# Performance work log

Hardware: AMD Instinct MI355X
Metric: run time of the kernel (lower is better)

Reference implementation:

```python
import jax, jax.numpy as jnp
import numpy as np

N_NODES = 10000
DEG = 32          # random neighbors per node; +1 self loop (A + I in original)
BATCH = 2
F_IN = 128
D_EMB = 128


def _make_edges():
    # np.where on a dense (A+I) matrix yields edges sorted by source row;
    # we build the same sorted-by-src edge list directly.
    rng = np.random.default_rng(0)
    src = np.repeat(np.arange(N_NODES), DEG + 1)
    dst = rng.integers(0, N_NODES, size=N_NODES * (DEG + 1))
    dst[DEG::DEG + 1] = np.arange(N_NODES)  # guarantee self loops
    return np.stack([src, dst], axis=1).astype(np.int32)  # [E, 2]


def setup_inputs() -> dict:
    key = jax.random.key(0)
    k1, k2, k3 = jax.random.split(key, 3)
    inputs = jax.random.normal(k1, (BATCH, N_NODES, F_IN), jnp.float32)
    W = jax.random.normal(k2, (F_IN, D_EMB), jnp.float32) * 0.1
    W_attn = jax.random.normal(k3, (2 * D_EMB, 1), jnp.float32) * 0.1
    edges = jnp.asarray(_make_edges())
    return {"inputs": inputs, "W": W, "W_attn": W_attn, "edges": edges}


def reference(inputs, W, W_attn, edges):
    # inputs: [B, N, F]; W: [F, D]; W_attn: [2D, 1]; edges: [E, 2] (sorted by src)
    B, N, _ = inputs.shape
    D = W.shape[1]
    src, dst = edges[:, 0], edges[:, 1]

    h = inputs @ W  # [B, N, D] node_states_transformed

    # Original: gather [src,dst] feats, reshape to [B,E,2D], matmul W_attn.
    # Equivalent efficient form: split W_attn and project per node first.
    a_src, a_dst = W_attn[:D, 0], W_attn[D:, 0]
    s = h @ a_src  # [B, N]
    d = h @ a_dst  # [B, N]
    scores = jax.nn.leaky_relu(s[:, src] + d[:, dst], negative_slope=0.2)  # [B, E]
    scores = jnp.exp(jnp.clip(scores, -2.0, 2.0))

    # Faithful to original bug: denominator uses batch 0 only, shared across batch.
    denom = jax.ops.segment_sum(scores[0], src, num_segments=N)  # [N]
    # edges sorted by src => tf.repeat(denom, bincount(src)) == denom[src]
    attn = scores / denom[src][None, :]  # [B, E]

    msgs = h[:, dst] * attn[:, :, None]  # [B, E, D]
    # tf.unsorted_segment_sum with rank-2 segment_ids sums over batch AND edges.
    out = jax.ops.segment_sum(msgs.sum(axis=0), src, num_segments=N)  # [N, D]
    return jnp.broadcast_to(out[None], (B, N, D))
```

## Files before the change

kernel.cpp:

```cpp
#include <hip/hip_runtime.h>
#include <math.h>

#define N_NODES 10000
#define DEG1 33
#define D_EMB 128
#define F_IN 128
#define BATCH 2

typedef short s8v  __attribute__((ext_vector_type(8)));
typedef float f4v  __attribute__((ext_vector_type(4)));

static __device__ __forceinline__ unsigned short f2bf(float f) {
    unsigned int x = __float_as_uint(f);
    unsigned int r = (x + 0x7fffu + ((x >> 16) & 1u)) >> 16;
    return (unsigned short)r;
}
static __device__ __forceinline__ float bf_lo(unsigned int u) { return __uint_as_float(u << 16); }
static __device__ __forceinline__ float bf_hi(unsigned int u) { return __uint_as_float(u & 0xffff0000u); }
static __device__ __forceinline__ float rdlane_f(float v, int l) {
    return __uint_as_float((unsigned int)__builtin_amdgcn_readlane((int)__float_as_uint(v), l));
}

__global__ __launch_bounds__(256) void gat_prep_kernel(
    const float* __restrict__ W, unsigned short* __restrict__ wtf)
{
    const int c = blockIdx.x;
    const int t = threadIdx.x;
    __shared__ float xs[128 * 16];
    #pragma unroll
    for (int r = 0; r < 8; ++r) {
        const int k = r * 16 + (t >> 4);
        const int n = t & 15;
        xs[k * 16 + n] = W[k * 128 + c * 16 + n];
    }
    __syncthreads();
    const int s = t >> 6;
    const int l = t & 63;
    s8v frag;
    #pragma unroll
    for (int j = 0; j < 8; ++j) {
        const int k = s * 32 + (l >> 4) * 8 + j;
        frag[j] = (short)f2bf(xs[k * 16 + (l & 15)]);
    }
    *(s8v*)&wtf[(((size_t)c * 4 + s) * 64 + l) * 8] = frag;
}

__global__ __launch_bounds__(256) void gat_h_kernel(
    const float* __restrict__ X, const unsigned short* __restrict__ wtf,
    const float* __restrict__ Wattn,
    unsigned short* __restrict__ hb, float* __restrict__ s_arr, float* __restrict__ d_arr)
{
    const int w = blockIdx.x * 4 + (threadIdx.x >> 6);
    if (w >= (BATCH * N_NODES) / 16) return;
    const int lane = threadIdx.x & 63;
    const int quad = lane >> 4;
    const int mrow = lane & 15;
    const int row0 = w * 16;

    f4v acc[8];
    #pragma unroll
    for (int c = 0; c < 8; ++c) acc[c] = (f4v){0.f, 0.f, 0.f, 0.f};

    const float* xrow = X + (size_t)(row0 + mrow) * F_IN;
    #pragma unroll
    for (int s = 0; s < 4; ++s) {
        const int k0 = s * 32 + quad * 8;
        const float4 xa = *(const float4*)&xrow[k0];
        const float4 xbv = *(const float4*)&xrow[k0 + 4];
        s8v a;
        a[0] = (short)f2bf(xa.x);  a[1] = (short)f2bf(xa.y);
        a[2] = (short)f2bf(xa.z);  a[3] = (short)f2bf(xa.w);
        a[4] = (short)f2bf(xbv.x); a[5] = (short)f2bf(xbv.y);
        a[6] = (short)f2bf(xbv.z); a[7] = (short)f2bf(xbv.w);
        #pragma unroll
        for (int c = 0; c < 8; ++c) {
            const s8v b = *(const s8v*)&wtf[(((size_t)c * 4 + s) * 64 + lane) * 8];
            acc[c] = __builtin_amdgcn_mfma_f32_16x16x32_bf16(a, b, acc[c], 0, 0, 0);
        }
    }

    const int b = (row0 >= N_NODES) ? 1 : 0;
    #pragma unroll
    for (int r = 0; r < 4; ++r) {
        const int R = row0 + quad * 4 + r;
        const int n = R - b * N_NODES;
        unsigned short* dst = &hb[((size_t)n * 2 + b) * D_EMB + mrow];
        #pragma unroll
        for (int c = 0; c < 8; ++c)
            dst[c * 16] = f2bf(acc[c][r]);
    }

    float as[8], ad[8];
    #pragma unroll
    for (int c = 0; c < 8; ++c) {
        as[c] = Wattn[c * 16 + mrow];
        ad[c] = Wattn[D_EMB + c * 16 + mrow];
    }
    #pragma unroll
    for (int r = 0; r < 4; ++r) {
        float sv = 0.f, dv = 0.f;
        #pragma unroll
        for (int c = 0; c < 8; ++c) {
            sv = fmaf(acc[c][r], as[c], sv);
            dv = fmaf(acc[c][r], ad[c], dv);
        }
        #pragma unroll
        for (int off = 1; off < 16; off <<= 1) {
            sv += __shfl_xor(sv, off, 16);
            dv += __shfl_xor(dv, off, 16);
        }
        if (mrow == 0) {
            const int R = row0 + quad * 4 + r;
            s_arr[R] = sv;
            d_arr[R] = dv;
        }
    }
}

__global__ __launch_bounds__(256) void gat_agg_kernel(
    const uint2* __restrict__ h2, const float* __restrict__ s_arr,
    const float* __restrict__ d_arr, const int* __restrict__ edges,
    float* __restrict__ out)
{
    const int i = blockIdx.x * 4 + (threadIdx.x >> 6);
    const int lane = threadIdx.x & 63;

    int dstv = 0; float sc0 = 0.f, sc1 = 0.f;
    if (lane < DEG1) {
        dstv = edges[((size_t)i * DEG1 + lane) * 2 + 1];
        float x0 = s_arr[i] + d_arr[dstv];
        float x1 = s_arr[N_NODES + i] + d_arr[N_NODES + dstv];
        x0 = (x0 >= 0.f) ? x0 : 0.2f * x0;
        x1 = (x1 >= 0.f) ? x1 : 0.2f * x1;
        sc0 = __expf(fminf(fmaxf(x0, -2.f), 2.f));
        sc1 = __expf(fminf(fmaxf(x1, -2.f), 2.f));
    }
    float dsum = sc0;
    #pragma unroll
    for (int off = 1; off < 64; off <<= 1) dsum += __shfl_xor(dsum, off, 64);
    const float inv = 1.f / dsum;
    sc0 *= inv;
    sc1 *= inv;

    float4 acc = make_float4(0.f, 0.f, 0.f, 0.f);
    #pragma unroll
    for (int j = 0; j < DEG1; ++j) {
        const int   dd = __builtin_amdgcn_readlane(dstv, j);
        const float w0 = rdlane_f(sc0, j);
        const float w1 = rdlane_f(sc1, j);
        const float wgt = (lane < 32) ? w0 : w1;
        const uint2 hv = h2[(size_t)dd * 64 + lane];
        acc.x = fmaf(wgt, bf_lo(hv.x), acc.x);
        acc.y = fmaf(wgt, bf_hi(hv.x), acc.y);
        acc.z = fmaf(wgt, bf_lo(hv.y), acc.z);
        acc.w = fmaf(wgt, bf_hi(hv.y), acc.w);
    }
    float4 o;
    o.x = acc.x + __shfl_xor(acc.x, 32, 64);
    o.y = acc.y + __shfl_xor(acc.y, 32, 64);
    o.z = acc.z + __shfl_xor(acc.z, 32, 64);
    o.w = acc.w + __shfl_xor(acc.w, 32, 64);

    const int b  = lane >> 5;
    const int dl = lane & 31;
    *(float4*)&out[((size_t)b * N_NODES + i) * D_EMB + dl * 4] = o;
}

extern "C" void kernel_launch(void* const* d_in, const int* in_sizes, int n_in,
                              void* d_out, int out_size, void* d_ws, size_t ws_size,
                              hipStream_t stream) {
    const float* X     = (const float*)d_in[0];
    const float* W     = (const float*)d_in[1];
    const float* Wattn = (const float*)d_in[2];
    const int*   edges = (const int*)d_in[3];
    float* out = (float*)d_out;

    unsigned short* wtf = (unsigned short*)d_ws;
    unsigned short* hb  = wtf + 16384;
    float* s_arr = (float*)(hb + (size_t)BATCH * N_NODES * D_EMB);
    float* d_arr = s_arr + BATCH * N_NODES;

    gat_prep_kernel<<<8, 256, 0, stream>>>(W, wtf);
    gat_h_kernel<<<313, 256, 0, stream>>>(X, wtf, Wattn, hb, s_arr, d_arr);
    gat_agg_kernel<<<N_NODES / 4, 256, 0, stream>>>((const uint2*)hb, s_arr, d_arr, edges, out);
}
```

Before: 90.52 us.

## Split feature table into column halves and aggregate in two passes

The bf16 node-feature table is now written as two separate tables, one per 64-column half. Aggregation runs as two launches, each gathering neighbor rows from one half-table and writing its half of the output columns. The aim is to shrink the randomly gathered working set per pass so it fits better in the per-XCD L2 cache. In exchange, edge loading, attention-score computation and softmax normalisation are done twice, each gather moves only 4 bytes per lane, and there is an extra kernel launch.

```diff
diff --git a/kernel.cpp b/kernel.cpp
--- a/kernel.cpp
+++ b/kernel.cpp
@@ -48,7 +48,8 @@
 __global__ __launch_bounds__(256) void gat_h_kernel(
     const float* __restrict__ X, const unsigned short* __restrict__ wtf,
     const float* __restrict__ Wattn,
-    unsigned short* __restrict__ hb, float* __restrict__ s_arr, float* __restrict__ d_arr)
+    unsigned short* __restrict__ hbA, unsigned short* __restrict__ hbB,
+    float* __restrict__ s_arr, float* __restrict__ d_arr)
 {
     const int w = blockIdx.x * 4 + (threadIdx.x >> 6);
     if (w >= (BATCH * N_NODES) / 16) return;
@@ -84,10 +85,12 @@
     for (int r = 0; r < 4; ++r) {
         const int R = row0 + quad * 4 + r;
         const int n = R - b * N_NODES;
-        unsigned short* dst = &hb[((size_t)n * 2 + b) * D_EMB + mrow];
+        const size_t base = ((size_t)n * 2 + b) * 64 + mrow;
         #pragma unroll
-        for (int c = 0; c < 8; ++c)
-            dst[c * 16] = f2bf(acc[c][r]);
+        for (int c = 0; c < 8; ++c) {
+            unsigned short* tab = (c < 4) ? hbA : hbB;
+            tab[base + (c & 3) * 16] = f2bf(acc[c][r]);
+        }
     }
 
     float as[8], ad[8];
@@ -117,10 +120,10 @@
     }
 }
 
-__global__ __launch_bounds__(256) void gat_agg_kernel(
-    const uint2* __restrict__ h2, const float* __restrict__ s_arr,
-    const float* __restrict__ d_arr, const int* __restrict__ edges,
-    float* __restrict__ out)
+__global__ __launch_bounds__(256) void gat_agg_half_kernel(
+    const unsigned int* __restrict__ tab,
+    const float* __restrict__ s_arr, const float* __restrict__ d_arr,
+    const int* __restrict__ edges, float* __restrict__ out, const int half)
 {
     const int i = blockIdx.x * 4 + (threadIdx.x >> 6);
     const int lane = threadIdx.x & 63;
@@ -142,28 +145,25 @@
     sc0 *= inv;
     sc1 *= inv;
 
-    float4 acc = make_float4(0.f, 0.f, 0.f, 0.f);
+    const int b  = lane >> 5;
+    const int dl = lane & 31;
+    float2 acc = make_float2(0.f, 0.f);
     #pragma unroll
     for (int j = 0; j < DEG1; ++j) {
         const int   dd = __builtin_amdgcn_readlane(dstv, j);
         const float w0 = rdlane_f(sc0, j);
         const float w1 = rdlane_f(sc1, j);
         const float wgt = (lane < 32) ? w0 : w1;
-        const uint2 hv = h2[(size_t)dd * 64 + lane];
-        acc.x = fmaf(wgt, bf_lo(hv.x), acc.x);
-        acc.y = fmaf(wgt, bf_hi(hv.x), acc.y);
-        acc.z = fmaf(wgt, bf_lo(hv.y), acc.z);
-        acc.w = fmaf(wgt, bf_hi(hv.y), acc.w);
+        const unsigned int u = tab[(((size_t)dd * 2 + b) << 5) + dl];
+        acc.x = fmaf(wgt, bf_lo(u), acc.x);
+        acc.y = fmaf(wgt, bf_hi(u), acc.y);
     }
-    float4 o;
+    float2 o;
     o.x = acc.x + __shfl_xor(acc.x, 32, 64);
     o.y = acc.y + __shfl_xor(acc.y, 32, 64);
-    o.z = acc.z + __shfl_xor(acc.z, 32, 64);
-    o.w = acc.w + __shfl_xor(acc.w, 32, 64);
 
-    const int b  = lane >> 5;
-    const int dl = lane & 31;
-    *(float4*)&out[((size_t)b * N_NODES + i) * D_EMB + dl * 4] = o;
+    float2* out2 = (float2*)out;
+    out2[((size_t)b * N_NODES + i) * (D_EMB / 2) + half * 32 + dl] = o;
 }
 
 extern "C" void kernel_launch(void* const* d_in, const int* in_sizes, int n_in,
@@ -176,11 +176,15 @@
     float* out = (float*)d_out;
 
     unsigned short* wtf = (unsigned short*)d_ws;
-    unsigned short* hb  = wtf + 16384;
-    float* s_arr = (float*)(hb + (size_t)BATCH * N_NODES * D_EMB);
+    unsigned short* hbA = wtf + 16384;
+    unsigned short* hbB = hbA + (size_t)BATCH * N_NODES * 64;
+    float* s_arr = (float*)(hbB + (size_t)BATCH * N_NODES * 64);
     float* d_arr = s_arr + BATCH * N_NODES;
 
     gat_prep_kernel<<<8, 256, 0, stream>>>(W, wtf);
-    gat_h_kernel<<<313, 256, 0, stream>>>(X, wtf, Wattn, hb, s_arr, d_arr);
-    gat_agg_kernel<<<N_NODES / 4, 256, 0, stream>>>((const uint2*)hb, s_arr, d_arr, edges, out);
+    gat_h_kernel<<<313, 256, 0, stream>>>(X, wtf, Wattn, hbA, hbB, s_arr, d_arr);
+    gat_agg_half_kernel<<<N_NODES / 4, 256, 0, stream>>>(
+        (const unsigned int*)hbA, s_arr, d_arr, edges, out, 0);
+    gat_agg_half_kernel<<<N_NODES / 4, 256, 0, stream>>>(
+        (const unsigned int*)hbB, s_arr, d_arr, edges, out, 1);
 }
```

Result: slower. 94.43 us (+4.3%).
